# Performance work log

Measured on AMD Instinct MI355X. Metric: run time of the kernel, lower is better.

Reference implementation:

```python
import jax, jax.numpy as jnp
import numpy as np

N = 100000   # nodes
E = 1600000  # edges
D = 64       # hidden_channels
H = 2 * D    # MLP expansion
L = 4        # num_layers
G = 64       # graphs in batch
OUT = 1      # out_channels
LN_EPS = 1e-5


def layer_norm(h, gamma, beta):
    mu = jnp.mean(h, axis=-1, keepdims=True)
    var = jnp.var(h, axis=-1, keepdims=True)
    return (h - mu) * jax.lax.rsqrt(var + LN_EPS) * gamma + beta


def setup_inputs() -> dict:
    key = jax.random.key(0)
    ks = jax.random.split(key, 16)
    s = 0.05
    x = jax.random.normal(ks[0], (N, D), jnp.float32)
    edge_index = jax.random.randint(ks[1], (2, E), 0, N)
    batch = jnp.sort(jax.random.randint(ks[2], (N,), 0, G))
    # lin_in
    W_in = jax.random.normal(ks[3], (D, D), jnp.float32) * s
    b_in = jnp.zeros((D,), jnp.float32)
    # per-layer GINConv params (stacked over L layers)
    eps = jnp.zeros((L,), jnp.float32)
    W1 = jax.random.normal(ks[4], (L, D, H), jnp.float32) * s
    b1 = jnp.zeros((L, H), jnp.float32)
    gamma = jnp.ones((L, H), jnp.float32)
    beta = jnp.zeros((L, H), jnp.float32)
    W2 = jax.random.normal(ks[5], (L, H, D), jnp.float32) * s
    b2 = jnp.zeros((L, D), jnp.float32)
    # lin_out MLP
    Wo1 = jax.random.normal(ks[6], (D, H), jnp.float32) * s
    bo1 = jnp.zeros((H,), jnp.float32)
    Wo2 = jax.random.normal(ks[7], (H, OUT), jnp.float32) * s
    bo2 = jnp.zeros((OUT,), jnp.float32)
    return {
        "x": x, "W_in": W_in, "b_in": b_in, "eps": eps,
        "W1": W1, "b1": b1, "gamma": gamma, "beta": beta,
        "W2": W2, "b2": b2, "Wo1": Wo1, "bo1": bo1,
        "Wo2": Wo2, "bo2": bo2,
        "edge_index": edge_index, "batch": batch,
    }


def gin_conv(h, edge_index, eps_l, W1_l, b1_l, gamma_l, beta_l, W2_l, b2_l):
    src = edge_index[0]  # x_j
    dst = edge_index[1]  # aggregation target i
    # message = relu(x_j); aggr = scatter-add into dst
    agg = jax.ops.segment_sum(jax.nn.relu(h[src]), dst, num_segments=N)
    z = (1.0 + eps_l) * h + agg
    z = z @ W1_l + b1_l
    z = jax.nn.relu(layer_norm(z, gamma_l, beta_l))
    return z @ W2_l + b2_l


def reference(x, W_in, b_in, eps, W1, b1, gamma, beta, W2, b2,
              Wo1, bo1, Wo2, bo2, edge_index, batch):
    h = x @ W_in + b_in  # [N, D]
    for i in range(L):
        h = h + gin_conv(h, edge_index, eps[i], W1[i], b1[i],
                         gamma[i], beta[i], W2[i], b2[i])
        # dropout p=0.0 -> identity
    pooled = jax.ops.segment_sum(h, batch, num_segments=G)  # [G, D]
    out = jax.nn.relu(pooled @ Wo1 + bo1) @ Wo2 + bo2        # [G, OUT]
    return out.reshape(-1)
```

## Files before the change

### kernel.cpp

```cpp
#include <hip/hip_runtime.h>
#include <hip/hip_bf16.h>

#define NN 100000
#define NE 1600000
#define DD 64
#define HH 128
#define NLAYERS 4
#define NGRAPH 64
#define NBUCKET 782
#define NCHUNK 391
#define NTOT (NBUCKET * NCHUNK)

typedef __attribute__((ext_vector_type(8))) short bf16x8;
typedef __attribute__((ext_vector_type(4))) float f32x4;

__device__ inline unsigned short bf16bits(float v) {
  return __bfloat16_as_ushort(__float2bfloat16(v));
}
__device__ inline float lo16(unsigned int u) { return __uint_as_float(u << 16); }
__device__ inline float hi16(unsigned int u) { return __uint_as_float(u & 0xFFFF0000u); }
__device__ inline float b2f(unsigned short u) { return __uint_as_float(((unsigned int)u) << 16); }


__global__ void k_hist(const int* __restrict__ dst, int* __restrict__ hist) {
  __shared__ int lh[NBUCKET];
  int t = threadIdx.x;
  int blk = blockIdx.x;
  for (int i = t; i < NBUCKET; i += 256) lh[i] = 0;
  __syncthreads();
  int cb = blk * 4096;
  int end = min(cb + 4096, NE);
  for (int i = cb + t; i < end; i += 256)
    atomicAdd(&lh[dst[i] >> 7], 1);
  __syncthreads();
  for (int i = t; i < NBUCKET; i += 256)
    hist[i * NCHUNK + blk] = lh[i];
}

__global__ void k_scan1(const int* __restrict__ in, int* __restrict__ out,
                        int* __restrict__ bsum, int n) {
  __shared__ int s[256];
  int t = threadIdx.x;
  int i = blockIdx.x * 256 + t;
  int v = (i < n) ? in[i] : 0;
  s[t] = v;
  __syncthreads();
  for (int off = 1; off < 256; off <<= 1) {
    int x = (t >= off) ? s[t - off] : 0;
    __syncthreads();
    s[t] += x;
    __syncthreads();
  }
  if (i < n) out[i] = s[t] - v;
  if (t == 255) bsum[blockIdx.x] = s[255];
}

__global__ void k_scan2b(int* bsum, int nb) {
  __shared__ int s[256];
  int t = threadIdx.x;
  int base = t * 5;
  int v[5];
  int sum = 0;
#pragma unroll
  for (int j = 0; j < 5; j++) {
    int i = base + j;
    v[j] = (i < nb) ? bsum[i] : 0;
    sum += v[j];
  }
  s[t] = sum;
  __syncthreads();
  for (int off = 1; off < 256; off <<= 1) {
    int x = (t >= off) ? s[t - off] : 0;
    __syncthreads();
    s[t] += x;
    __syncthreads();
  }
  int ex = s[t] - sum;
#pragma unroll
  for (int j = 0; j < 5; j++) {
    int i = base + j;
    if (i < nb) { int vv = v[j]; bsum[i] = ex; ex += vv; }
  }
}

__global__ void k_scan3b(int* __restrict__ hist, const int* __restrict__ bsum,
                         int* __restrict__ bbase, int n) {
  int i = blockIdx.x * 256 + threadIdx.x;
  if (i < n) {
    int v = hist[i] + bsum[i >> 8];
    hist[i] = v;
    if (i % NCHUNK == 0) bbase[i / NCHUNK] = v;
  }
}

__global__ void k_scatter(const int* __restrict__ src, const int* __restrict__ dst,
                          const int* __restrict__ hist, unsigned int* __restrict__ tmp) {
  __shared__ int lcur[NBUCKET];
  int t = threadIdx.x;
  int blk = blockIdx.x;
  for (int i = t; i < NBUCKET; i += 256) lcur[i] = hist[i * NCHUNK + blk];
  __syncthreads();
  int cb = blk * 4096;
  int end = min(cb + 4096, NE);
  for (int i = cb + t; i < end; i += 256) {
    int d = dst[i];
    int pos = atomicAdd(&lcur[d >> 7], 1);
    tmp[pos] = ((unsigned int)(d & 127) << 20) | (unsigned int)src[i];
  }
}

__global__ void k_fillB2(const unsigned int* __restrict__ tmp,
                         const int* __restrict__ bbase,
                         int* __restrict__ csr, int* __restrict__ offs,
                         int* __restrict__ cnt) {
  __shared__ int lcnt[128], lex[128], lcur[128];
  int b = blockIdx.x;
  int t = threadIdx.x;
  int base = bbase[b];
  int end = (b == NBUCKET - 1) ? NE : bbase[b + 1];
  if (t < 128) lcnt[t] = 0;
  __syncthreads();
  for (int i = base + t; i < end; i += 256)
    atomicAdd(&lcnt[tmp[i] >> 20], 1);
  __syncthreads();
  int v = (t < 128) ? lcnt[t] : 0;
  if (t < 128) lex[t] = v;
  __syncthreads();
  for (int off = 1; off < 128; off <<= 1) {
    int x = (t >= off && t < 128) ? lex[t - off] : 0;
    __syncthreads();
    if (t < 128) lex[t] += x;
    __syncthreads();
  }
  if (t < 128) {
    int ex = lex[t] - v;
    lcur[t] = ex;
    int node = (b << 7) + t;
    if (node < NN) { offs[node] = base + ex; cnt[node] = v; }
  }
  __syncthreads();
  for (int i = base + t; i < end; i += 256) {
    unsigned int u = tmp[i];
    int dl = u >> 20;
    int pos = atomicAdd(&lcur[dl], 1);
    csr[base + pos] = u & 0xFFFFF;
  }
}

__global__ void k_prep(const float* __restrict__ W1, const float* __restrict__ W2,
                       const float* __restrict__ W_in,
                       unsigned short* __restrict__ W1t, unsigned short* __restrict__ W2t,
                       unsigned short* __restrict__ Wint) {
  int bidx = blockIdx.x;
  int t = threadIdx.x;
  if (bidx == 2 * NLAYERS) {
    for (int i = t; i < 4096; i += 256) {
      int c = i >> 6, k = i & 63;
      Wint[i] = bf16bits(W_in[k * 64 + c]);
    }
    return;
  }
  int l = bidx >> 1;
  int m = bidx & 1;
  if (m == 0) {
    const float* src = W1 + (size_t)l * 8192;
    unsigned short* dstp = W1t + (size_t)l * 8192;
    for (int i = t; i < 8192; i += 256) {
      int c = i >> 6, k = i & 63;
      dstp[i] = bf16bits(src[k * 128 + c]);
    }
  } else {
    const float* src = W2 + (size_t)l * 8192;
    unsigned short* dstp = W2t + (size_t)l * 8192;
    for (int i = t; i < 8192; i += 256) {
      int c = i >> 7, k = i & 127;
      dstp[i] = bf16bits(src[k * 64 + c]);
    }
  }
}

__global__ __launch_bounds__(256) void k_lin(
    const float* __restrict__ x, const unsigned short* __restrict__ Wint,
    const float* __restrict__ binp, unsigned short* __restrict__ hout) {
  __shared__ __align__(16) unsigned short sW[4096];
  __shared__ float sb[64];
  int t = threadIdx.x;
  {
    const uint4* wg = (const uint4*)Wint;
    uint4* sWu = (uint4*)sW;
    for (int g = t; g < 512; g += 256) {
      int c = g >> 3, s = g & 7;
      sWu[c * 8 + (s ^ (c & 7))] = wg[g];
    }
    if (t < 64) sb[t] = binp[t];
  }
  int l = t & 63, w = t >> 6, lm = l & 15, lk = l >> 4;
  int rowl = w * 16 + lm;
  int grow = blockIdx.x * 64 + rowl;
  int growc = min(grow, NN - 1);
  bf16x8 a[2];
#pragma unroll
  for (int kb = 0; kb < 2; kb++) {
    const float* xp = &x[(size_t)growc * 64 + kb * 32 + lk * 8];
    float4 x0 = *(const float4*)xp;
    float4 x1 = *(const float4*)(xp + 4);
    a[kb][0] = (short)bf16bits(x0.x); a[kb][1] = (short)bf16bits(x0.y);
    a[kb][2] = (short)bf16bits(x0.z); a[kb][3] = (short)bf16bits(x0.w);
    a[kb][4] = (short)bf16bits(x1.x); a[kb][5] = (short)bf16bits(x1.y);
    a[kb][6] = (short)bf16bits(x1.z); a[kb][7] = (short)bf16bits(x1.w);
  }
  __syncthreads();
  f32x4 acc[4];
#pragma unroll
  for (int n = 0; n < 4; n++) {
    float bc = sb[n * 16 + lm];
    acc[n] = (f32x4){bc, bc, bc, bc};
  }
  const bf16x8* sWf = (const bf16x8*)sW;
#pragma unroll
  for (int n = 0; n < 4; n++) {
    int c = n * 16 + lm;
    bf16x8 b0 = sWf[c * 8 + ((0 * 4 + lk) ^ (c & 7))];
    bf16x8 b1 = sWf[c * 8 + ((1 * 4 + lk) ^ (c & 7))];
    acc[n] = __builtin_amdgcn_mfma_f32_16x16x32_bf16(a[0], b0, acc[n], 0, 0, 0);
    acc[n] = __builtin_amdgcn_mfma_f32_16x16x32_bf16(a[1], b1, acc[n], 0, 0, 0);
  }
#pragma unroll
  for (int r = 0; r < 4; r++) {
    int grow2 = blockIdx.x * 64 + w * 16 + lk * 4 + r;
    if (grow2 < NN) {
#pragma unroll
      for (int n = 0; n < 4; n++) {
        int c = n * 16 + lm;
        hout[(size_t)grow2 * 64 + c] = bf16bits(acc[n][r]);
      }
    }
  }
}

__global__ __launch_bounds__(256) void k_fused(
    const unsigned short* __restrict__ hin, unsigned short* __restrict__ hout,
    const int* __restrict__ csr, const int* __restrict__ offs,
    const int* __restrict__ cnt,
    const unsigned short* __restrict__ W1t, const float* __restrict__ b1l,
    const float* __restrict__ gl, const float* __restrict__ btl,
    const unsigned short* __restrict__ W2t, const float* __restrict__ b2l,
    const float* __restrict__ epsl) {
  __shared__ __align__(16) unsigned short sW[8192];
  __shared__ __align__(16) unsigned short sRr[8192];
  __shared__ float sb1[128], sg[128], sbt[128], sb2[64];

  int t = threadIdx.x;
  int nbase = blockIdx.x * 64;
  int l = t & 63;
  int w = t >> 6;
  int lm = l & 15;
  int lk = l >> 4;

  {
    const uint4* w1g = (const uint4*)W1t;
    uint4* sWu = (uint4*)sW;
    for (int g = t; g < 1024; g += 256) {
      int c = g >> 3, s = g & 7;
      sWu[c * 8 + (s ^ (c & 7))] = w1g[g];
    }
    if (t < 128) { sb1[t] = b1l[t]; sg[t] = gl[t]; sbt[t] = btl[t]; }
    if (t < 64) sb2[t] = b2l[t];
  }
  float epsv = 1.0f + *epsl;

  int rowl = w * 16 + lm;
  int grow = nbase + rowl;
  int growc = min(grow, NN - 1);
  int start = offs[growc];
  int deg = (grow < NN) ? cnt[growc] : 0;

  const unsigned short* hp = hin + (size_t)growc * 64 + lk * 8;
  uint4 hva = *(const uint4*)hp;
  uint4 hvb = *(const uint4*)(hp + 32);

  float accA[8] = {0.f, 0.f, 0.f, 0.f, 0.f, 0.f, 0.f, 0.f};
  float accB[8] = {0.f, 0.f, 0.f, 0.f, 0.f, 0.f, 0.f, 0.f};
  for (int j0 = 0; j0 < deg; j0 += 8) {
    int idxA = csr[start + j0 + lk];
    int idxB = csr[start + j0 + 4 + lk];
    int c8 = deg - j0;
    int ss[8];
#pragma unroll
    for (int jj = 0; jj < 4; jj++) ss[jj] = __shfl(idxA, lm + jj * 16);
#pragma unroll
    for (int jj = 0; jj < 4; jj++) ss[4 + jj] = __shfl(idxB, lm + jj * 16);
    uint4 va[8], vb[8];
#pragma unroll
    for (int jj = 0; jj < 8; jj++) {
      int s = (jj < c8) ? ss[jj] : ss[0];
      const unsigned short* rp = hin + (size_t)s * 64 + lk * 8;
      va[jj] = *(const uint4*)rp;
      vb[jj] = *(const uint4*)(rp + 32);
    }
#pragma unroll
    for (int jj = 0; jj < 8; jj++) {
      if (jj < c8) {
        uint4 vA = va[jj], vB = vb[jj];
        accA[0] += fmaxf(lo16(vA.x), 0.f);
        accA[1] += fmaxf(hi16(vA.x), 0.f);
        accA[2] += fmaxf(lo16(vA.y), 0.f);
        accA[3] += fmaxf(hi16(vA.y), 0.f);
        accA[4] += fmaxf(lo16(vA.z), 0.f);
        accA[5] += fmaxf(hi16(vA.z), 0.f);
        accA[6] += fmaxf(lo16(vA.w), 0.f);
        accA[7] += fmaxf(hi16(vA.w), 0.f);
        accB[0] += fmaxf(lo16(vB.x), 0.f);
        accB[1] += fmaxf(hi16(vB.x), 0.f);
        accB[2] += fmaxf(lo16(vB.y), 0.f);
        accB[3] += fmaxf(hi16(vB.y), 0.f);
        accB[4] += fmaxf(lo16(vB.z), 0.f);
        accB[5] += fmaxf(hi16(vB.z), 0.f);
        accB[6] += fmaxf(lo16(vB.w), 0.f);
        accB[7] += fmaxf(hi16(vB.w), 0.f);
      }
    }
  }

  bf16x8 a1[2];
  {
    float hz[8];
    hz[0] = lo16(hva.x); hz[1] = hi16(hva.x); hz[2] = lo16(hva.y); hz[3] = hi16(hva.y);
    hz[4] = lo16(hva.z); hz[5] = hi16(hva.z); hz[6] = lo16(hva.w); hz[7] = hi16(hva.w);
#pragma unroll
    for (int j = 0; j < 8; j++) a1[0][j] = (short)bf16bits(epsv * hz[j] + accA[j]);
    hz[0] = lo16(hvb.x); hz[1] = hi16(hvb.x); hz[2] = lo16(hvb.y); hz[3] = hi16(hvb.y);
    hz[4] = lo16(hvb.z); hz[5] = hi16(hvb.z); hz[6] = lo16(hvb.w); hz[7] = hi16(hvb.w);
#pragma unroll
    for (int j = 0; j < 8; j++) a1[1][j] = (short)bf16bits(epsv * hz[j] + accB[j]);
  }
  __syncthreads();

  f32x4 acc1[8];
#pragma unroll
  for (int n = 0; n < 8; n++) {
    float bc = sb1[n * 16 + lm];
    acc1[n] = (f32x4){bc, bc, bc, bc};
  }
  {
    const bf16x8* sW1f = (const bf16x8*)sW;
#pragma unroll
    for (int n = 0; n < 8; n++) {
      int c = n * 16 + lm;
      bf16x8 b0 = sW1f[c * 8 + ((0 * 4 + lk) ^ (c & 7))];
      bf16x8 b1f = sW1f[c * 8 + ((1 * 4 + lk) ^ (c & 7))];
      acc1[n] = __builtin_amdgcn_mfma_f32_16x16x32_bf16(a1[0], b0, acc1[n], 0, 0, 0);
      acc1[n] = __builtin_amdgcn_mfma_f32_16x16x32_bf16(a1[1], b1f, acc1[n], 0, 0, 0);
    }
  }

  float psr[4], pqr[4];
#pragma unroll
  for (int r = 0; r < 4; r++) {
    float s = 0.f, q = 0.f;
#pragma unroll
    for (int n = 0; n < 8; n++) { float v = acc1[n][r]; s += v; q += v * v; }
    psr[r] = s; pqr[r] = q;
  }
#pragma unroll
  for (int m = 1; m <= 8; m <<= 1) {
#pragma unroll
    for (int r = 0; r < 4; r++) {
      psr[r] += __shfl_xor(psr[r], m);
      pqr[r] += __shfl_xor(pqr[r], m);
    }
  }
#pragma unroll
  for (int r = 0; r < 4; r++) {
    float mu = psr[r] * (1.0f / 128.0f);
    float var = pqr[r] * (1.0f / 128.0f) - mu * mu;
    float rs = rsqrtf(var + 1e-5f);
    int rowr = w * 16 + lk * 4 + r;
#pragma unroll
    for (int n = 0; n < 8; n++) {
      int c = n * 16 + lm;
      float v = (acc1[n][r] - mu) * rs * sg[c] + sbt[c];
      v = fmaxf(v, 0.f);
      int slot = (c >> 3) ^ (rowr & 7);
      sRr[rowr * 128 + slot * 8 + (c & 7)] = bf16bits(v);
    }
  }
  __syncthreads();

  {
    const uint4* w2g = (const uint4*)W2t;
    uint4* sWu = (uint4*)sW;
    for (int g = t; g < 1024; g += 256) {
      int c = g >> 4, s = g & 15;
      sWu[c * 16 + (s ^ (c & 15))] = w2g[g];
    }
  }
  __syncthreads();

  f32x4 acc2[4];
#pragma unroll
  for (int n2 = 0; n2 < 4; n2++) {
    float bc = sb2[n2 * 16 + lm];
    acc2[n2] = (f32x4){bc, bc, bc, bc};
  }
  {
    const bf16x8* sRf = (const bf16x8*)sRr;
    const bf16x8* sW2f = (const bf16x8*)sW;
    bf16x8 a2[4];
#pragma unroll
    for (int kb = 0; kb < 4; kb++)
      a2[kb] = sRf[rowl * 16 + ((kb * 4 + lk) ^ (rowl & 7))];
#pragma unroll
    for (int n2 = 0; n2 < 4; n2++) {
      int c = n2 * 16 + lm;
#pragma unroll
      for (int kb = 0; kb < 4; kb++) {
        bf16x8 bfr = sW2f[c * 16 + ((kb * 4 + lk) ^ (c & 15))];
        acc2[n2] = __builtin_amdgcn_mfma_f32_16x16x32_bf16(a2[kb], bfr, acc2[n2], 0, 0, 0);
      }
    }
  }

#pragma unroll
  for (int r = 0; r < 4; r++) {
    int grow2 = nbase + w * 16 + lk * 4 + r;
    if (grow2 < NN) {
#pragma unroll
      for (int n2 = 0; n2 < 4; n2++) {
        int c = n2 * 16 + lm;
        size_t idx = (size_t)grow2 * 64 + c;
        float o = b2f(hin[idx]) + acc2[n2][r];
        hout[idx] = bf16bits(o);
      }
    }
  }
}

__global__ void k_pool(const unsigned short* __restrict__ h,
                       const int* __restrict__ batch,
                       float* __restrict__ pooled, int n) {
  int t = threadIdx.x;
  int d = t & 63;
  int w = t >> 6;
  int n0 = blockIdx.x * 256 + w * 64;
  float acc = 0.f;
  int prev = -1;
  for (int i = 0; i < 64; i++) {
    int nn = n0 + i;
    if (nn >= n) break;
    int g = batch[nn];
    if (g != prev) {
      if (prev >= 0) atomicAdd(&pooled[prev * 64 + d], acc);
      prev = g;
      acc = 0.f;
    }
    acc += b2f(h[(size_t)nn * 64 + d]);
  }
  if (prev >= 0) atomicAdd(&pooled[prev * 64 + d], acc);
}

__global__ __launch_bounds__(128) void k_out(
    const float* __restrict__ pooled, const float* __restrict__ Wo1,
    const float* __restrict__ bo1, const float* __restrict__ Wo2,
    const float* __restrict__ bo2, float* __restrict__ out) {
  __shared__ __align__(16) float sP[64];
  __shared__ float sPart[2];
  int g = blockIdx.x;
  int c = threadIdx.x;
  if (c < 64) sP[c] = pooled[g * 64 + c];
  __syncthreads();
  float t1 = bo1[c];
#pragma unroll 8
  for (int k = 0; k < 64; k++) t1 += sP[k] * Wo1[k * 128 + c];
  float v = fmaxf(t1, 0.f) * Wo2[c];
#pragma unroll
  for (int m = 1; m <= 32; m <<= 1) v += __shfl_xor(v, m);
  if ((c & 63) == 0) sPart[c >> 6] = v;
  __syncthreads();
  if (c == 0) out[g] = sPart[0] + sPart[1] + bo2[0];
}


static inline char* align_up(char* p, size_t a) {
  return (char*)(((uintptr_t)p + a - 1) & ~(uintptr_t)(a - 1));
}

extern "C" void kernel_launch(void* const* d_in, const int* in_sizes, int n_in,
                              void* d_out, int out_size, void* d_ws, size_t ws_size,
                              hipStream_t stream) {
  const float* x    = (const float*)d_in[0];
  const float* W_in = (const float*)d_in[1];
  const float* b_in = (const float*)d_in[2];
  const float* eps  = (const float*)d_in[3];
  const float* W1   = (const float*)d_in[4];
  const float* b1   = (const float*)d_in[5];
  const float* gam  = (const float*)d_in[6];
  const float* bet  = (const float*)d_in[7];
  const float* W2   = (const float*)d_in[8];
  const float* b2   = (const float*)d_in[9];
  const float* Wo1  = (const float*)d_in[10];
  const float* bo1  = (const float*)d_in[11];
  const float* Wo2  = (const float*)d_in[12];
  const float* bo2  = (const float*)d_in[13];
  const int* ei     = (const int*)d_in[14];
  const int* batch  = (const int*)d_in[15];
  float* out = (float*)d_out;

  const int* e_src = ei;
  const int* e_dst = ei + NE;

  char* p = (char*)d_ws;
  unsigned short* hA = (unsigned short*)p;  p += (size_t)NN * 64 * 2;
  unsigned short* hB = (unsigned short*)p;
  unsigned int* tmp = (unsigned int*)p;
                                            p += (size_t)NN * 64 * 2;
  int* csr = (int*)p;
  int* hist = (int*)p;
                                            p += (size_t)NE * 4;
  int* offs = (int*)p;                      p += (size_t)NN * 4;
  int* cnt = (int*)p;                       p += (size_t)NN * 4;
  int* bsumH = (int*)p;                     p += 1280 * 4;
  int* bbase = (int*)p;                     p += (NBUCKET + 1) * 4;
  p = align_up(p, 256);
  float* pooled = (float*)p;                p += (size_t)NGRAPH * 64 * 4;
  p = align_up(p, 256);
  unsigned short* W1t = (unsigned short*)p; p += (size_t)NLAYERS * 8192 * 2;
  unsigned short* W2t = (unsigned short*)p; p += (size_t)NLAYERS * 8192 * 2;
  unsigned short* Wint = (unsigned short*)p; p += 4096 * 2;

  const int SCAN_BLOCKS_H = (NTOT + 255) / 256;
  const int NODE_BLOCKS = (NN + 63) / 64;

  hipMemsetAsync(pooled, 0, (size_t)NGRAPH * 64 * 4, stream);

  k_hist<<<NCHUNK, 256, 0, stream>>>(e_dst, hist);
  k_scan1<<<SCAN_BLOCKS_H, 256, 0, stream>>>(hist, hist, bsumH, NTOT);
  k_scan2b<<<1, 256, 0, stream>>>(bsumH, SCAN_BLOCKS_H);
  k_scan3b<<<SCAN_BLOCKS_H, 256, 0, stream>>>(hist, bsumH, bbase, NTOT);
  k_scatter<<<NCHUNK, 256, 0, stream>>>(e_src, e_dst, hist, tmp);
  k_fillB2<<<NBUCKET, 256, 0, stream>>>(tmp, bbase, csr, offs, cnt);

  k_prep<<<NLAYERS * 2 + 1, 256, 0, stream>>>(W1, W2, W_in, W1t, W2t, Wint);
  k_lin<<<NODE_BLOCKS, 256, 0, stream>>>(x, Wint, b_in, hA);

  for (int l = 0; l < NLAYERS; l++) {
    const unsigned short* hin = (l & 1) ? hB : hA;
    unsigned short* ho = (l & 1) ? hA : hB;
    k_fused<<<NODE_BLOCKS, 256, 0, stream>>>(hin, ho, csr, offs, cnt,
        W1t + (size_t)l * 8192, b1 + (size_t)l * 128,
        gam + (size_t)l * 128, bet + (size_t)l * 128,
        W2t + (size_t)l * 8192, b2 + (size_t)l * 64,
        eps + l);
  }

  k_pool<<<(NN + 255) / 256, 256, 0, stream>>>(hA, batch, pooled, NN);
  k_out<<<NGRAPH, 128, 0, stream>>>(pooled, Wo1, bo1, Wo2, bo2, out);
}
```

Measured before the change: 339.6 us.

## Gather neighbor features from precomputed FP8 ReLU copy and update h in place

Adds a per-layer pass that applies ReLU to the bf16 node features and packs them into FP8, so the edge gather in the fused layer kernel reads 8 bytes per half-row instead of 16. The point is to cut the gather traffic, which dominates the aggregation. The double buffer is replaced by a single h updated in place, which works because each block reads only its own rows' self term and residual. The cost is an extra conversion kernel per layer and FP8 rounding of the aggregated messages, which may affect accuracy tolerance.

```diff
diff --git a/kernel.cpp b/kernel.cpp
--- a/kernel.cpp
+++ b/kernel.cpp
@@ -13,6 +13,7 @@
 
 typedef __attribute__((ext_vector_type(8))) short bf16x8;
 typedef __attribute__((ext_vector_type(4))) float f32x4;
+typedef __attribute__((ext_vector_type(2))) float f32x2;
 
 __device__ inline unsigned short bf16bits(float v) {
   return __bfloat16_as_ushort(__float2bfloat16(v));
@@ -238,8 +239,28 @@
   }
 }
 
+__global__ __launch_bounds__(256) void k_f8(const unsigned short* __restrict__ h,
+                                            uint2* __restrict__ f8) {
+  int i = blockIdx.x * 256 + threadIdx.x;
+  if (i >= NN * 8) return;
+  uint4 v = ((const uint4*)h)[i];
+  float d0 = fmaxf(lo16(v.x), 0.f), d1 = fmaxf(hi16(v.x), 0.f);
+  float d2 = fmaxf(lo16(v.y), 0.f), d3 = fmaxf(hi16(v.y), 0.f);
+  float d4 = fmaxf(lo16(v.z), 0.f), d5 = fmaxf(hi16(v.z), 0.f);
+  float d6 = fmaxf(lo16(v.w), 0.f), d7 = fmaxf(hi16(v.w), 0.f);
+  int lo = 0, hi = 0;
+  lo = __builtin_amdgcn_cvt_pk_fp8_f32(d0, d1, lo, false);
+  lo = __builtin_amdgcn_cvt_pk_fp8_f32(d2, d3, lo, true);
+  hi = __builtin_amdgcn_cvt_pk_fp8_f32(d4, d5, hi, false);
+  hi = __builtin_amdgcn_cvt_pk_fp8_f32(d6, d7, hi, true);
+  uint2 o;
+  o.x = (unsigned int)lo;
+  o.y = (unsigned int)hi;
+  f8[i] = o;
+}
+
 __global__ __launch_bounds__(256) void k_fused(
-    const unsigned short* __restrict__ hin, unsigned short* __restrict__ hout,
+    unsigned short* __restrict__ h, const uint2* __restrict__ f8v,
     const int* __restrict__ csr, const int* __restrict__ offs,
     const int* __restrict__ cnt,
     const unsigned short* __restrict__ W1t, const float* __restrict__ b1l,
@@ -275,7 +296,7 @@
   int start = offs[growc];
   int deg = (grow < NN) ? cnt[growc] : 0;
 
-  const unsigned short* hp = hin + (size_t)growc * 64 + lk * 8;
+  const unsigned short* hp = h + (size_t)growc * 64 + lk * 8;
   uint4 hva = *(const uint4*)hp;
   uint4 hvb = *(const uint4*)(hp + 32);
 
@@ -290,34 +311,25 @@
     for (int jj = 0; jj < 4; jj++) ss[jj] = __shfl(idxA, lm + jj * 16);
 #pragma unroll
     for (int jj = 0; jj < 4; jj++) ss[4 + jj] = __shfl(idxB, lm + jj * 16);
-    uint4 va[8], vb[8];
+    uint2 va[8], vb[8];
 #pragma unroll
     for (int jj = 0; jj < 8; jj++) {
       int s = (jj < c8) ? ss[jj] : ss[0];
-      const unsigned short* rp = hin + (size_t)s * 64 + lk * 8;
-      va[jj] = *(const uint4*)rp;
-      vb[jj] = *(const uint4*)(rp + 32);
+      va[jj] = f8v[(size_t)s * 8 + lk];
+      vb[jj] = f8v[(size_t)s * 8 + 4 + lk];
     }
 #pragma unroll
     for (int jj = 0; jj < 8; jj++) {
       if (jj < c8) {
-        uint4 vA = va[jj], vB = vb[jj];
-        accA[0] += fmaxf(lo16(vA.x), 0.f);
-        accA[1] += fmaxf(hi16(vA.x), 0.f);
-        accA[2] += fmaxf(lo16(vA.y), 0.f);
-        accA[3] += fmaxf(hi16(vA.y), 0.f);
-        accA[4] += fmaxf(lo16(vA.z), 0.f);
-        accA[5] += fmaxf(hi16(vA.z), 0.f);
-        accA[6] += fmaxf(lo16(vA.w), 0.f);
-        accA[7] += fmaxf(hi16(vA.w), 0.f);
-        accB[0] += fmaxf(lo16(vB.x), 0.f);
-        accB[1] += fmaxf(hi16(vB.x), 0.f);
-        accB[2] += fmaxf(lo16(vB.y), 0.f);
-        accB[3] += fmaxf(hi16(vB.y), 0.f);
-        accB[4] += fmaxf(lo16(vB.z), 0.f);
-        accB[5] += fmaxf(hi16(vB.z), 0.f);
-        accB[6] += fmaxf(lo16(vB.w), 0.f);
-        accB[7] += fmaxf(hi16(vB.w), 0.f);
+        f32x2 p;
+        p = __builtin_amdgcn_cvt_pk_f32_fp8(va[jj].x, false); accA[0] += p.x; accA[1] += p.y;
+        p = __builtin_amdgcn_cvt_pk_f32_fp8(va[jj].x, true);  accA[2] += p.x; accA[3] += p.y;
+        p = __builtin_amdgcn_cvt_pk_f32_fp8(va[jj].y, false); accA[4] += p.x; accA[5] += p.y;
+        p = __builtin_amdgcn_cvt_pk_f32_fp8(va[jj].y, true);  accA[6] += p.x; accA[7] += p.y;
+        p = __builtin_amdgcn_cvt_pk_f32_fp8(vb[jj].x, false); accB[0] += p.x; accB[1] += p.y;
+        p = __builtin_amdgcn_cvt_pk_f32_fp8(vb[jj].x, true);  accB[2] += p.x; accB[3] += p.y;
+        p = __builtin_amdgcn_cvt_pk_f32_fp8(vb[jj].y, false); accB[4] += p.x; accB[5] += p.y;
+        p = __builtin_amdgcn_cvt_pk_f32_fp8(vb[jj].y, true);  accB[6] += p.x; accB[7] += p.y;
       }
     }
   }
@@ -429,8 +441,8 @@
       for (int n2 = 0; n2 < 4; n2++) {
         int c = n2 * 16 + lm;
         size_t idx = (size_t)grow2 * 64 + c;
-        float o = b2f(hin[idx]) + acc2[n2][r];
-        hout[idx] = bf16bits(o);
+        float o = b2f(h[idx]) + acc2[n2][r];
+        h[idx] = bf16bits(o);
       }
     }
   }
@@ -510,10 +522,10 @@
   const int* e_dst = ei + NE;
 
   char* p = (char*)d_ws;
-  unsigned short* hA = (unsigned short*)p;  p += (size_t)NN * 64 * 2;
-  unsigned short* hB = (unsigned short*)p;
+  unsigned short* h = (unsigned short*)p;   p += (size_t)NN * 64 * 2;
+  uint2* f8 = (uint2*)p;
   unsigned int* tmp = (unsigned int*)p;
-                                            p += (size_t)NN * 64 * 2;
+                                            p += (size_t)NN * 64;
   int* csr = (int*)p;
   int* hist = (int*)p;
                                             p += (size_t)NE * 4;
@@ -530,6 +542,7 @@
 
   const int SCAN_BLOCKS_H = (NTOT + 255) / 256;
   const int NODE_BLOCKS = (NN + 63) / 64;
+  const int F8_BLOCKS = (NN * 8 + 255) / 256;
 
   hipMemsetAsync(pooled, 0, (size_t)NGRAPH * 64 * 4, stream);
 
@@ -541,18 +554,17 @@
   k_fillB2<<<NBUCKET, 256, 0, stream>>>(tmp, bbase, csr, offs, cnt);
 
   k_prep<<<NLAYERS * 2 + 1, 256, 0, stream>>>(W1, W2, W_in, W1t, W2t, Wint);
-  k_lin<<<NODE_BLOCKS, 256, 0, stream>>>(x, Wint, b_in, hA);
+  k_lin<<<NODE_BLOCKS, 256, 0, stream>>>(x, Wint, b_in, h);
 
   for (int l = 0; l < NLAYERS; l++) {
-    const unsigned short* hin = (l & 1) ? hB : hA;
-    unsigned short* ho = (l & 1) ? hA : hB;
-    k_fused<<<NODE_BLOCKS, 256, 0, stream>>>(hin, ho, csr, offs, cnt,
+    k_f8<<<F8_BLOCKS, 256, 0, stream>>>(h, f8);
+    k_fused<<<NODE_BLOCKS, 256, 0, stream>>>(h, f8, csr, offs, cnt,
         W1t + (size_t)l * 8192, b1 + (size_t)l * 128,
         gam + (size_t)l * 128, bet + (size_t)l * 128,
         W2t + (size_t)l * 8192, b2 + (size_t)l * 64,
         eps + l);
   }
 
-  k_pool<<<(NN + 255) / 256, 256, 0, stream>>>(hA, batch, pooled, NN);
+  k_pool<<<(NN + 255) / 256, 256, 0, stream>>>(h, batch, pooled, NN);
   k_out<<<NGRAPH, 128, 0, stream>>>(pooled, Wo1, bo1, Wo2, bo2, out);
 }
```

Measured after the change: 325.6 us. 1.04x faster.
